# Performance work log

Measured on AMD Instinct MI355X. Metric: run time of the kernel, lower is better.

Reference implementation:

```python
import jax, jax.numpy as jnp
import numpy as np

NUM_QUBIT = 23
N0 = 2
DIM = 2 ** NUM_QUBIT  # 8388608


def setup_inputs() -> dict:
    key = jax.random.key(0)
    ks = jax.random.split(key, 6)
    shape = (N0, DIM)
    code0_real = jax.random.normal(ks[0], shape, jnp.float32)
    code0_imag = jax.random.normal(ks[1], shape, jnp.float32)
    code1_real = jax.random.normal(ks[2], shape, jnp.float32)
    code1_imag = jax.random.normal(ks[3], shape, jnp.float32)
    # per-qubit 2x2 unitaries: random complex matrices, unitarized via QR
    ur = jax.random.normal(ks[4], (NUM_QUBIT, 2, 2), jnp.float32)
    ui = jax.random.normal(ks[5], (NUM_QUBIT, 2, 2), jnp.float32)
    q, _ = jnp.linalg.qr(ur + 1j * ui)  # [n,2,2] complex64 unitary
    return {
        "code0_real": code0_real,
        "code0_imag": code0_imag,
        "code1_real": code1_real,
        "code1_imag": code1_imag,
        "unitary_real": jnp.real(q).astype(jnp.float32),
        "unitary_imag": jnp.imag(q).astype(jnp.float32),
    }


def reference(code0_real, code0_imag, code1_real, code1_imag,
              unitary_real, unitary_imag):
    code0 = code0_real + 1j * code0_imag            # [N0, 2^n] complex64
    code1 = code1_real + 1j * code1_imag            # [N0, 2^n]
    unitary = unitary_real + 1j * unitary_imag      # [n, 2, 2]
    n = unitary.shape[0]
    n0 = code0.shape[0]
    # sequential per-qubit 2x2 gate application on the statevectors
    for ind0 in range(n):
        tmp0 = code0.reshape(n0 * 2 ** ind0, 2, -1)  # [N0*2^i, 2, 2^(n-i-1)]
        # out[a,d,c] = sum_b tmp0[a,b,c] * U[b,d]
        code0 = jnp.einsum('abc,bd->adc', tmp0, unitary[ind0]).reshape(n0, -1)
    overlap = (jnp.conj(code0) @ code1.T).reshape(-1)  # [N0*N0]
    loss = n0 - jnp.real(jnp.vdot(overlap, overlap))
    return loss
```

## Files before the change

kernel.cpp:

```cpp
#include <hip/hip_runtime.h>

#define DIM_ (1 << 23)
#define N0_ 2

__device__ float g_acc[8];

__device__ __forceinline__ int swz(int x) {
    return x ^ ((x >> 5) & 3) ^ (((x >> 7) & 7) << 2);
}

__device__ __forceinline__ void gload(const float* __restrict__ ur,
                                      const float* __restrict__ ui, int q,
                                      float2& u00, float2& u01, float2& u10, float2& u11) {
    u00 = make_float2(ur[q * 4 + 0], ui[q * 4 + 0]);
    u01 = make_float2(ur[q * 4 + 1], ui[q * 4 + 1]);
    u10 = make_float2(ur[q * 4 + 2], ui[q * 4 + 2]);
    u11 = make_float2(ur[q * 4 + 3], ui[q * 4 + 3]);
}

__device__ __forceinline__ void bfly(float2& a0, float2& a1,
                                     float2 u00, float2 u01, float2 u10, float2 u11) {
    float2 n0, n1;
    n0.x = a0.x * u00.x - a0.y * u00.y + a1.x * u10.x - a1.y * u10.y;
    n0.y = a0.x * u00.y + a0.y * u00.x + a1.x * u10.y + a1.y * u10.x;
    n1.x = a0.x * u01.x - a0.y * u01.y + a1.x * u11.x - a1.y * u11.y;
    n1.y = a0.x * u01.y + a0.y * u01.x + a1.x * u11.y + a1.y * u11.x;
    a0 = n0; a1 = n1;
}

#define BFLY16(S, Q)                                                           \
    do {                                                                       \
        float2 u00, u01, u10, u11;                                             \
        gload(ur, ui, (Q), u00, u01, u10, u11);                                \
        _Pragma("unroll")                                                      \
        for (int m0 = 0; m0 < 16; ++m0)                                        \
            if (!(m0 & (S))) bfly(v[m0], v[m0 + (S)], u00, u01, u10, u11);     \
    } while (0)

template <bool INTER>
__global__ __launch_bounds__(512, 2) void k_low(
    const float* __restrict__ inr, const float* __restrict__ ini,
    const float* __restrict__ ur, const float* __restrict__ ui,
    float2* __restrict__ outI, float* __restrict__ outR, float* __restrict__ outJ) {
    __shared__ float2 buf[8192];
    const int t = threadIdx.x;
    const int H = blockIdx.x;
    const int base = blockIdx.y * DIM_ + (H << 13);

    float2 v[16];
#pragma unroll
    for (int k = 0; k < 4; ++k) {
        const int y = (k << 11) | (t << 2);
        const float4 re = *(const float4*)(inr + base + y);
        const float4 im = *(const float4*)(ini + base + y);
        v[k * 4 + 0] = make_float2(re.x, im.x);
        v[k * 4 + 1] = make_float2(re.y, im.y);
        v[k * 4 + 2] = make_float2(re.z, im.z);
        v[k * 4 + 3] = make_float2(re.w, im.w);
    }
    BFLY16(1, 22);
    BFLY16(2, 21);
    BFLY16(4, 11);
    BFLY16(8, 10);
#pragma unroll
    for (int m = 0; m < 16; ++m)
        buf[swz(((m >> 2) << 11) | (t << 2) | (m & 3))] = v[m];
    __syncthreads();
#pragma unroll
    for (int m = 0; m < 16; ++m)
        v[m] = buf[swz((t & 3) | (m << 2) | ((t >> 2) << 6))];
    BFLY16(1, 20);
    BFLY16(2, 19);
    BFLY16(4, 18);
    BFLY16(8, 17);
#pragma unroll
    for (int m = 0; m < 16; ++m)
        buf[swz((t & 3) | (m << 2) | ((t >> 2) << 6))] = v[m];
    __syncthreads();
#pragma unroll
    for (int m = 0; m < 16; ++m)
        v[m] = buf[swz((t & 63) | (m << 6) | ((t >> 6) << 10))];
    BFLY16(1, 16);
    BFLY16(2, 15);
    BFLY16(4, 14);
    BFLY16(8, 13);
#pragma unroll
    for (int m = 0; m < 16; ++m)
        buf[swz((t & 63) | (m << 6) | ((t >> 6) << 10))] = v[m];
    __syncthreads();
    {
        float2 u00, u01, u10, u11;
        gload(ur, ui, 12, u00, u01, u10, u11);
#pragma unroll
        for (int rp = 0; rp < 4; ++rp) {
            const int x0 = (rp << 11) | (t << 1);
            float2 a0 = buf[swz(x0)];
            float2 a1 = buf[swz(x0 | 1)];
            float2 b0 = buf[swz(x0 | 1024)];
            float2 b1 = buf[swz(x0 | 1025)];
            bfly(a0, b0, u00, u01, u10, u11);
            bfly(a1, b1, u00, u01, u10, u11);
            if (INTER) {
                const int l0 = x0, l1 = x0 | 1024;
                const int o0 = ((l0 >> 3) << 13) | (H << 3) | (l0 & 7);
                const int o1 = ((l1 >> 3) << 13) | (H << 3) | (l1 & 7);
                float2* p = outI + blockIdx.y * DIM_;
                *(float4*)(p + o0) = make_float4(a0.x, a0.y, a1.x, a1.y);
                *(float4*)(p + o1) = make_float4(b0.x, b0.y, b1.x, b1.y);
            } else {
                *(float2*)(outR + base + x0) = make_float2(a0.x, a1.x);
                *(float2*)(outJ + base + x0) = make_float2(a0.y, a1.y);
                *(float2*)(outR + base + (x0 | 1024)) = make_float2(b0.x, b1.x);
                *(float2*)(outJ + base + (x0 | 1024)) = make_float2(b0.y, b1.y);
            }
        }
    }
}

template <bool INTER>
__device__ __forceinline__ void high_pass(
    float2 (&v)[16], float2* buf, const int t, const int g, const int i,
    const float2* __restrict__ wsI, const float* __restrict__ wsR,
    const float* __restrict__ wsJ,
    const float* __restrict__ ur, const float* __restrict__ ui) {
    if constexpr (INTER) {
        const float4* wsv = (const float4*)(wsI + i * DIM_ + (g << 13));
#pragma unroll
        for (int k = 0; k < 4; ++k)
#pragma unroll
            for (int jh = 0; jh < 2; ++jh) {
                const float4 f = wsv[(k << 10) | (t << 1) | jh];
                v[k * 4 + jh * 2 + 0] = make_float2(f.x, f.y);
                v[k * 4 + jh * 2 + 1] = make_float2(f.z, f.w);
            }
    } else {
#pragma unroll
        for (int k = 0; k < 4; ++k) {
            const int y0 = (k << 11) | (t << 2);
            const int a = ((y0 >> 3) << 13) | (g << 3) | (y0 & 7);
            const float4 re = *(const float4*)(wsR + i * DIM_ + a);
            const float4 im = *(const float4*)(wsJ + i * DIM_ + a);
            v[k * 4 + 0] = make_float2(re.x, im.x);
            v[k * 4 + 1] = make_float2(re.y, im.y);
            v[k * 4 + 2] = make_float2(re.z, im.z);
            v[k * 4 + 3] = make_float2(re.w, im.w);
        }
    }
    BFLY16(4, 1);
    BFLY16(8, 0);
#pragma unroll
    for (int m = 0; m < 16; ++m)
        buf[swz(((m >> 2) << 11) | (t << 2) | (m & 3))] = v[m];
    __syncthreads();
#pragma unroll
    for (int m = 0; m < 16; ++m)
        v[m] = buf[swz((t & 7) | (m << 3) | ((t >> 3) << 7))];
    BFLY16(1, 9);
    BFLY16(2, 8);
    BFLY16(4, 7);
    BFLY16(8, 6);
#pragma unroll
    for (int m = 0; m < 16; ++m)
        buf[swz((t & 7) | (m << 3) | ((t >> 3) << 7))] = v[m];
    __syncthreads();
#pragma unroll
    for (int m = 0; m < 16; ++m)
        v[m] = buf[swz((t & 127) | (m << 7) | ((t >> 7) << 11))];
    BFLY16(1, 5);
    BFLY16(2, 4);
    BFLY16(4, 3);
    BFLY16(8, 2);
}

template <bool INTER>
__global__ __launch_bounds__(512, 2) void k_high(
    const float2* __restrict__ wsI, const float* __restrict__ wsR, const float* __restrict__ wsJ,
    const float* __restrict__ c1r, const float* __restrict__ c1i,
    const float* __restrict__ ur, const float* __restrict__ ui) {
    __shared__ float2 buf[8192];
    const int t = threadIdx.x;
    const int g = blockIdx.x;
    float acc[8];
#pragma unroll
    for (int k = 0; k < 8; ++k) acc[k] = 0.f;

    float2 v0[16], v1[16];
    high_pass<INTER>(v0, buf, t, g, 0, wsI, wsR, wsJ, ur, ui);
    __syncthreads();
    high_pass<INTER>(v1, buf, t, g, 1, wsI, wsR, wsJ, ur, ui);

#pragma unroll
    for (int m = 0; m < 16; ++m) {
        const int y = (t & 127) | (m << 7) | ((t >> 7) << 11);
        const int idx = ((y >> 3) << 13) | (g << 3) | (y & 7);
        const float ar = c1r[idx], ai = c1i[idx];
        const float br = c1r[DIM_ + idx], bi = c1i[DIM_ + idx];
        acc[0] += v0[m].x * ar + v0[m].y * ai;
        acc[1] += v0[m].x * ai - v0[m].y * ar;
        acc[2] += v0[m].x * br + v0[m].y * bi;
        acc[3] += v0[m].x * bi - v0[m].y * br;
        acc[4] += v1[m].x * ar + v1[m].y * ai;
        acc[5] += v1[m].x * ai - v1[m].y * ar;
        acc[6] += v1[m].x * br + v1[m].y * bi;
        acc[7] += v1[m].x * bi - v1[m].y * br;
    }

#pragma unroll
    for (int k = 0; k < 8; ++k)
#pragma unroll
        for (int off = 32; off > 0; off >>= 1)
            acc[k] += __shfl_down(acc[k], off, 64);
    __syncthreads();
    float* red = (float*)buf;
    const int wave = t >> 6, lane = t & 63;
    if (lane == 0) {
#pragma unroll
        for (int k = 0; k < 8; ++k) red[wave * 8 + k] = acc[k];
    }
    __syncthreads();
    if (t < 8) {
        float s = 0.f;
#pragma unroll
        for (int w = 0; w < 8; ++w) s += red[w * 8 + t];
        atomicAdd(&g_acc[t], s);
    }
}

__global__ void k_zero() {
    if (threadIdx.x < 8) g_acc[threadIdx.x] = 0.f;
}

__global__ void k_fin(float* __restrict__ out) {
    if (threadIdx.x == 0) {
        float s = 0.f;
#pragma unroll
        for (int k = 0; k < 4; ++k)
            s += g_acc[2 * k] * g_acc[2 * k] + g_acc[2 * k + 1] * g_acc[2 * k + 1];
        out[0] = (float)N0_ - s;
    }
}

extern "C" void kernel_launch(void* const* d_in, const int* in_sizes, int n_in,
                              void* d_out, int out_size, void* d_ws, size_t ws_size,
                              hipStream_t stream) {
    const float* c0r = (const float*)d_in[0];
    const float* c0i = (const float*)d_in[1];
    const float* c1r = (const float*)d_in[2];
    const float* c1i = (const float*)d_in[3];
    const float* ur  = (const float*)d_in[4];
    const float* ui  = (const float*)d_in[5];
    float* out = (float*)d_out;

    const size_t need = (size_t)N0_ * DIM_ * sizeof(float2);
    k_zero<<<1, 64, 0, stream>>>();
    dim3 g1(1024, N0_);
    if (d_ws != nullptr && ws_size >= need) {
        float2* wsI = (float2*)d_ws;
        k_low<true><<<g1, 512, 0, stream>>>(c0r, c0i, ur, ui, wsI, nullptr, nullptr);
        k_high<true><<<1024, 512, 0, stream>>>(wsI, nullptr, nullptr, c1r, c1i, ur, ui);
    } else {
        float* oR = (float*)c0r;
        float* oJ = (float*)c0i;
        k_low<false><<<g1, 512, 0, stream>>>(c0r, c0i, ur, ui, nullptr, oR, oJ);
        k_high<false><<<1024, 512, 0, stream>>>(nullptr, oR, oJ, c1r, c1i, ur, ui);
    }
    k_fin<<<1, 64, 0, stream>>>(out);
}
```

Before: 417.4 us.

## Prefetch second statevector and interleave dot products in high-qubit kernel

The high-qubit kernel now issues the global loads for the second statevector before the first statevector's overlap dot-product pass, so that load latency overlaps with compute. The dot product for each statevector is done right after its transform, which lowers live register pressure compared with holding both vectors at once. Block indices are permuted so that neighbouring blocks touch strided column groups, and nontemporal loads are used for streaming inputs. The added prefetch buffer costs registers, and the nontemporal hints may change cache behaviour for data that is read again.

```diff
diff --git a/kernel.cpp b/kernel.cpp
--- a/kernel.cpp
+++ b/kernel.cpp
@@ -2,6 +2,8 @@
 
 #define DIM_ (1 << 23)
 #define N0_ 2
+
+typedef float f32x4 __attribute__((ext_vector_type(4)));
 
 __device__ float g_acc[8];
 
@@ -51,8 +53,8 @@
 #pragma unroll
     for (int k = 0; k < 4; ++k) {
         const int y = (k << 11) | (t << 2);
-        const float4 re = *(const float4*)(inr + base + y);
-        const float4 im = *(const float4*)(ini + base + y);
+        const f32x4 re = __builtin_nontemporal_load((const f32x4*)(inr + base + y));
+        const f32x4 im = __builtin_nontemporal_load((const f32x4*)(ini + base + y));
         v[k * 4 + 0] = make_float2(re.x, im.x);
         v[k * 4 + 1] = make_float2(re.y, im.y);
         v[k * 4 + 2] = make_float2(re.z, im.z);
@@ -118,34 +120,56 @@
 }
 
 template <bool INTER>
-__device__ __forceinline__ void high_pass(
-    float2 (&v)[16], float2* buf, const int t, const int g, const int i,
-    const float2* __restrict__ wsI, const float* __restrict__ wsR,
-    const float* __restrict__ wsJ,
-    const float* __restrict__ ur, const float* __restrict__ ui) {
+__device__ __forceinline__ void load_ws(f32x4 (&raw)[8], const int t, const int g, const int i,
+                                        const float2* __restrict__ wsI,
+                                        const float* __restrict__ wsR,
+                                        const float* __restrict__ wsJ) {
     if constexpr (INTER) {
-        const float4* wsv = (const float4*)(wsI + i * DIM_ + (g << 13));
+        const f32x4* wsv = (const f32x4*)(wsI + i * DIM_ + (g << 13));
 #pragma unroll
         for (int k = 0; k < 4; ++k)
 #pragma unroll
+            for (int jh = 0; jh < 2; ++jh)
+                raw[k * 2 + jh] =
+                    __builtin_nontemporal_load(wsv + ((k << 10) | (t << 1) | jh));
+    } else {
+#pragma unroll
+        for (int k = 0; k < 4; ++k) {
+            const int y0 = (k << 11) | (t << 2);
+            const int a = ((y0 >> 3) << 13) | (g << 3) | (y0 & 7);
+            raw[k * 2 + 0] = *(const f32x4*)(wsR + i * DIM_ + a);
+            raw[k * 2 + 1] = *(const f32x4*)(wsJ + i * DIM_ + a);
+        }
+    }
+}
+
+template <bool INTER>
+__device__ __forceinline__ void unpack_ws(const f32x4 (&raw)[8], float2 (&v)[16]) {
+    if constexpr (INTER) {
+#pragma unroll
+        for (int k = 0; k < 4; ++k)
+#pragma unroll
             for (int jh = 0; jh < 2; ++jh) {
-                const float4 f = wsv[(k << 10) | (t << 1) | jh];
+                const f32x4 f = raw[k * 2 + jh];
                 v[k * 4 + jh * 2 + 0] = make_float2(f.x, f.y);
                 v[k * 4 + jh * 2 + 1] = make_float2(f.z, f.w);
             }
     } else {
 #pragma unroll
         for (int k = 0; k < 4; ++k) {
-            const int y0 = (k << 11) | (t << 2);
-            const int a = ((y0 >> 3) << 13) | (g << 3) | (y0 & 7);
-            const float4 re = *(const float4*)(wsR + i * DIM_ + a);
-            const float4 im = *(const float4*)(wsJ + i * DIM_ + a);
+            const f32x4 re = raw[k * 2 + 0];
+            const f32x4 im = raw[k * 2 + 1];
             v[k * 4 + 0] = make_float2(re.x, im.x);
             v[k * 4 + 1] = make_float2(re.y, im.y);
             v[k * 4 + 2] = make_float2(re.z, im.z);
             v[k * 4 + 3] = make_float2(re.w, im.w);
         }
     }
+}
+
+__device__ __forceinline__ void high_transform(float2 (&v)[16], float2* buf, const int t,
+                                               const float* __restrict__ ur,
+                                               const float* __restrict__ ui) {
     BFLY16(4, 1);
     BFLY16(8, 0);
 #pragma unroll
@@ -170,6 +194,24 @@
     BFLY16(2, 4);
     BFLY16(4, 3);
     BFLY16(8, 2);
+}
+
+template <int J0>
+__device__ __forceinline__ void dot_pass(const float2 (&v)[16], float (&acc)[8],
+                                         const int t, const int g,
+                                         const float* __restrict__ c1r,
+                                         const float* __restrict__ c1i) {
+#pragma unroll
+    for (int m = 0; m < 16; ++m) {
+        const int y = (t & 127) | (m << 7) | ((t >> 7) << 11);
+        const int idx = ((y >> 3) << 13) | (g << 3) | (y & 7);
+        const float ar = c1r[idx], ai = c1i[idx];
+        const float br = c1r[DIM_ + idx], bi = c1i[DIM_ + idx];
+        acc[J0 + 0] += v[m].x * ar + v[m].y * ai;
+        acc[J0 + 1] += v[m].x * ai - v[m].y * ar;
+        acc[J0 + 2] += v[m].x * br + v[m].y * bi;
+        acc[J0 + 3] += v[m].x * bi - v[m].y * br;
+    }
 }
 
 template <bool INTER>
@@ -179,31 +221,26 @@
     const float* __restrict__ ur, const float* __restrict__ ui) {
     __shared__ float2 buf[8192];
     const int t = threadIdx.x;
-    const int g = blockIdx.x;
+    const int b = blockIdx.x;
+    const int g = ((b & 7) << 7) | (b >> 3);
     float acc[8];
 #pragma unroll
     for (int k = 0; k < 8; ++k) acc[k] = 0.f;
 
-    float2 v0[16], v1[16];
-    high_pass<INTER>(v0, buf, t, g, 0, wsI, wsR, wsJ, ur, ui);
-    __syncthreads();
-    high_pass<INTER>(v1, buf, t, g, 1, wsI, wsR, wsJ, ur, ui);
-
-#pragma unroll
-    for (int m = 0; m < 16; ++m) {
-        const int y = (t & 127) | (m << 7) | ((t >> 7) << 11);
-        const int idx = ((y >> 3) << 13) | (g << 3) | (y & 7);
-        const float ar = c1r[idx], ai = c1i[idx];
-        const float br = c1r[DIM_ + idx], bi = c1i[DIM_ + idx];
-        acc[0] += v0[m].x * ar + v0[m].y * ai;
-        acc[1] += v0[m].x * ai - v0[m].y * ar;
-        acc[2] += v0[m].x * br + v0[m].y * bi;
-        acc[3] += v0[m].x * bi - v0[m].y * br;
-        acc[4] += v1[m].x * ar + v1[m].y * ai;
-        acc[5] += v1[m].x * ai - v1[m].y * ar;
-        acc[6] += v1[m].x * br + v1[m].y * bi;
-        acc[7] += v1[m].x * bi - v1[m].y * br;
-    }
+    f32x4 raw[8];
+    float2 v0[16];
+    load_ws<INTER>(raw, t, g, 0, wsI, wsR, wsJ);
+    unpack_ws<INTER>(raw, v0);
+    high_transform(v0, buf, t, ur, ui);
+    load_ws<INTER>(raw, t, g, 1, wsI, wsR, wsJ);
+    dot_pass<0>(v0, acc, t, g, c1r, c1i);
+
+    __syncthreads();
+
+    float2 v1[16];
+    unpack_ws<INTER>(raw, v1);
+    high_transform(v1, buf, t, ur, ui);
+    dot_pass<4>(v1, acc, t, g, c1r, c1i);
 
 #pragma unroll
     for (int k = 0; k < 8; ++k)
```

Result: slower. 434.1 us (+4.0%).
